# Kernel tuning notes

Hardware: AMD Instinct MI355X
Metric: run time of the kernel (lower is better)

The kernel has to match this reference:

```python
import jax, jax.numpy as jnp
import numpy as np

N, D = 4194304, 3  # points on S^2 embedded in R^3
STEPS = 100


def proj2tangent(x, v):
    # v - (<x,v>/<x,x>) x  : ambient projection onto tangent space at x
    dot = jnp.sum(x * v, axis=-1, keepdims=True)
    nrm2 = jnp.sum(x * x, axis=-1, keepdims=True)
    return v - (dot / nrm2) * x


def proj2manifold(x):
    return x / jnp.linalg.norm(x, axis=-1, keepdims=True)


def setup_inputs() -> dict:
    key = jax.random.key(0)
    x = jax.random.normal(key, (N, D), dtype=jnp.float32)
    x = proj2manifold(x)  # start on the sphere
    return {"x": x, "t": 1, "steps": STEPS}


def reference(x, t, steps):
    # Stratonovich-Heun integration of spherical Brownian motion.
    # drift f == 0; diffusion increment g(x, t, dW) = proj2tangent(x, dW).
    dt = t / steps
    sqrt_dt = jnp.sqrt(jnp.asarray(dt, dtype=x.dtype))
    base_key = jax.random.key(1)

    def step_fn(xc, i):
        inc = jax.random.normal(jax.random.fold_in(base_key, i), xc.shape, xc.dtype) * sqrt_dt
        g0 = proj2tangent(xc, inc)
        y_prime = xc + g0                     # f0 * dt == 0
        g_prime = proj2tangent(y_prime, inc)
        y1 = xc + 0.5 * (g0 + g_prime)        # 0.5*(f0+f')*dt == 0
        return proj2manifold(y1), None

    x_final, _ = jax.lax.scan(step_fn, x, jnp.arange(steps))
    return x_final
```

## Files before the change

kernel.cpp:

```cpp
#include <hip/hip_runtime.h>
#include <stdint.h>


#define BLOCK 256

struct V3 { float x, y, z; };

__device__ __forceinline__ void tf_round(uint32_t& x0, uint32_t& x1, int r) {
    x0 += x1;
    x1 = (x1 << r) | (x1 >> (32 - r));
    x1 ^= x0;
}

__device__ __forceinline__ uint2 threefry2x32(uint32_t k0, uint32_t k1,
                                              uint32_t x0, uint32_t x1) {
    uint32_t k2 = k0 ^ k1 ^ 0x1BD11BDAu;
    x0 += k0; x1 += k1;
    tf_round(x0,x1,13); tf_round(x0,x1,15); tf_round(x0,x1,26); tf_round(x0,x1,6);
    x0 += k1; x1 += k2 + 1u;
    tf_round(x0,x1,17); tf_round(x0,x1,29); tf_round(x0,x1,16); tf_round(x0,x1,24);
    x0 += k2; x1 += k0 + 2u;
    tf_round(x0,x1,13); tf_round(x0,x1,15); tf_round(x0,x1,26); tf_round(x0,x1,6);
    x0 += k0; x1 += k1 + 3u;
    tf_round(x0,x1,17); tf_round(x0,x1,29); tf_round(x0,x1,16); tf_round(x0,x1,24);
    x0 += k1; x1 += k2 + 4u;
    tf_round(x0,x1,13); tf_round(x0,x1,15); tf_round(x0,x1,26); tf_round(x0,x1,6);
    x0 += k2; x1 += k0 + 5u;
    return make_uint2(x0, x1);
}

__device__ __forceinline__ uint32_t tf_bits(uint32_t k0, uint32_t k1, uint32_t j) {
    uint2 h = threefry2x32(k0, k1, 0u, j);
    return h.x ^ h.y;
}

__device__ __forceinline__ float bits_to_inc(uint32_t bits, float c) {
    const float mn = -0.99999994f;
    float u01 = __uint_as_float((bits >> 9) | 0x3f800000u) - 1.0f;
    float u   = fmaf(u01, 2.0f, mn);
    float s   = u * u;
    float tt  = 1.0f - s;
    float w   = -__logf(tt);
    float wa  = w - 2.5f;
    float p =  2.81022636e-08f;
    p = fmaf(p, wa,  3.43273939e-07f);
    p = fmaf(p, wa, -3.5233877e-06f);
    p = fmaf(p, wa, -4.39150654e-06f);
    p = fmaf(p, wa,  0.00021858087f);
    p = fmaf(p, wa, -0.00125372503f);
    p = fmaf(p, wa, -0.00417768164f);
    p = fmaf(p, wa,  0.246640727f);
    p = fmaf(p, wa,  1.50140941f);
    if (__builtin_expect(__any(w >= 5.0f), 0)) {
        float wb = __builtin_amdgcn_sqrtf(w) - 3.0f;
        float q = -0.000200214257f;
        q = fmaf(q, wb,  0.000100950558f);
        q = fmaf(q, wb,  0.00134934322f);
        q = fmaf(q, wb, -0.00367342844f);
        q = fmaf(q, wb,  0.00573950773f);
        q = fmaf(q, wb, -0.0076224613f);
        q = fmaf(q, wb,  0.00943887047f);
        q = fmaf(q, wb,  1.00167406f);
        q = fmaf(q, wb,  2.83297682f);
        p = (w < 5.0f) ? p : q;
    }
    return (p * u) * c;
}

__device__ __forceinline__ float rcp_f(float a) { return __builtin_amdgcn_rcpf(a); }

__device__ __forceinline__ void heun_step(V3& p, V3 inc) {
    float d  = p.x*inc.x + p.y*inc.y + p.z*inc.z;
    float n2 = p.x*p.x + p.y*p.y + p.z*p.z;
    float q  = d * rcp_f(n2);
    V3 g0 = { inc.x - q*p.x, inc.y - q*p.y, inc.z - q*p.z };
    V3 yp = { p.x + g0.x, p.y + g0.y, p.z + g0.z };
    float d2 = yp.x*inc.x + yp.y*inc.y + yp.z*inc.z;
    float m2 = yp.x*yp.x + yp.y*yp.y + yp.z*yp.z;
    float q2 = d2 * rcp_f(m2);
    V3 gp = { inc.x - q2*yp.x, inc.y - q2*yp.y, inc.z - q2*yp.z };
    V3 y1 = { p.x + 0.5f*(g0.x+gp.x), p.y + 0.5f*(g0.y+gp.y), p.z + 0.5f*(g0.z+gp.z) };
    float r2   = y1.x*y1.x + y1.y*y1.y + y1.z*y1.z;
    float rinv = __builtin_amdgcn_rsqf(r2);
    p.x = y1.x * rinv; p.y = y1.y * rinv; p.z = y1.z * rinv;
}

__global__ __launch_bounds__(BLOCK)
void sbm_kernel(const float* __restrict__ xin,
                const int* __restrict__ t_ptr,
                const int* __restrict__ steps_ptr,
                float* __restrict__ out,
                uint32_t npts) {
    __shared__ uint2 skeys[128];

    const int steps = steps_ptr[0];
    const int tval  = t_ptr[0];
    const int tid   = threadIdx.x;

    if (tid < steps && tid < 128) skeys[tid] = threefry2x32(0u, 1u, 0u, (uint32_t)tid);
    __syncthreads();

    const float dt  = (float)((double)tval / (double)steps);
    const float sdt = sqrtf(dt);
    const float c   = 1.41421356237f * sdt;

    const uint32_t g = blockIdx.x * BLOCK + tid;
    if (g >= npts) return;

    const float* px = xin + 3u * g;
    V3 P = { px[0], px[1], px[2] };
    const uint32_t j0 = 3u * g;

    for (int i = 0; i < steps; ++i) {
        uint2 key = skeys[i & 127];
        uint32_t b0 = tf_bits(key.x, key.y, j0);
        uint32_t b1 = tf_bits(key.x, key.y, j0 + 1u);
        uint32_t b2 = tf_bits(key.x, key.y, j0 + 2u);
        V3 inc = { bits_to_inc(b0, c), bits_to_inc(b1, c), bits_to_inc(b2, c) };
        heun_step(P, inc);
    }

    float* po = out + 3u * g;
    po[0] = P.x; po[1] = P.y; po[2] = P.z;
}

extern "C" void kernel_launch(void* const* d_in, const int* in_sizes, int n_in,
                              void* d_out, int out_size, void* d_ws, size_t ws_size,
                              hipStream_t stream) {
    const float* x      = (const float*)d_in[0];
    const int*   t_ptr  = (const int*)d_in[1];
    const int*   steps  = (const int*)d_in[2];
    float*       out    = (float*)d_out;

    const uint32_t npts = (uint32_t)(in_sizes[0] / 3);
    const uint32_t grid = (npts + BLOCK - 1) / BLOCK;

    sbm_kernel<<<grid, BLOCK, 0, stream>>>(x, t_ptr, steps, out, npts);
}
```

Measured before the change: 2.836 ms.

## Process two points per thread, scalarize RNG keys, and simplify log and projection

Each thread now integrates two points, one from each half of the array, to expose more independent work per thread. The per-step Threefry key is broadcast with readfirstlane so the key arithmetic can live in scalar registers. The inverse-erf path uses log2 folded into an fma, and the first tangent projection drops the norm division on the assumption that the point is already unit length. This halves the thread count and silently leaves one point unprocessed if the point count is odd.

```diff
diff --git a/kernel.cpp b/kernel.cpp
--- a/kernel.cpp
+++ b/kernel.cpp
@@ -40,8 +40,9 @@
     float u   = fmaf(u01, 2.0f, mn);
     float s   = u * u;
     float tt  = 1.0f - s;
-    float w   = -__logf(tt);
-    float wa  = w - 2.5f;
+    float lg  = __log2f(tt);
+    const float nln2 = -0.69314718f;
+    float wa  = fmaf(lg, nln2, -2.5f);
     float p =  2.81022636e-08f;
     p = fmaf(p, wa,  3.43273939e-07f);
     p = fmaf(p, wa, -3.5233877e-06f);
@@ -51,7 +52,8 @@
     p = fmaf(p, wa, -0.00417768164f);
     p = fmaf(p, wa,  0.246640727f);
     p = fmaf(p, wa,  1.50140941f);
-    if (__builtin_expect(__any(w >= 5.0f), 0)) {
+    if (__builtin_expect(__any(lg <= -7.2134752f), 0)) {
+        float w  = lg * nln2;
         float wb = __builtin_amdgcn_sqrtf(w) - 3.0f;
         float q = -0.000200214257f;
         q = fmaf(q, wb,  0.000100950558f);
@@ -62,7 +64,7 @@
         q = fmaf(q, wb,  0.00943887047f);
         q = fmaf(q, wb,  1.00167406f);
         q = fmaf(q, wb,  2.83297682f);
-        p = (w < 5.0f) ? p : q;
+        p = (lg > -7.2134752f) ? p : q;
     }
     return (p * u) * c;
 }
@@ -71,9 +73,7 @@
 
 __device__ __forceinline__ void heun_step(V3& p, V3 inc) {
     float d  = p.x*inc.x + p.y*inc.y + p.z*inc.z;
-    float n2 = p.x*p.x + p.y*p.y + p.z*p.z;
-    float q  = d * rcp_f(n2);
-    V3 g0 = { inc.x - q*p.x, inc.y - q*p.y, inc.z - q*p.z };
+    V3 g0 = { inc.x - d*p.x, inc.y - d*p.y, inc.z - d*p.z };
     V3 yp = { p.x + g0.x, p.y + g0.y, p.z + g0.z };
     float d2 = yp.x*inc.x + yp.y*inc.y + yp.z*inc.z;
     float m2 = yp.x*yp.x + yp.y*yp.y + yp.z*yp.z;
@@ -90,7 +90,7 @@
                 const int* __restrict__ t_ptr,
                 const int* __restrict__ steps_ptr,
                 float* __restrict__ out,
-                uint32_t npts) {
+                uint32_t nhalf) {
     __shared__ uint2 skeys[128];
 
     const int steps = steps_ptr[0];
@@ -105,23 +105,35 @@
     const float c   = 1.41421356237f * sdt;
 
     const uint32_t g = blockIdx.x * BLOCK + tid;
-    if (g >= npts) return;
+    if (g >= nhalf) return;
 
-    const float* px = xin + 3u * g;
-    V3 P = { px[0], px[1], px[2] };
-    const uint32_t j0 = 3u * g;
+    const float* pa = xin + 3u * g;
+    const float* pb = xin + 3u * (g + nhalf);
+    V3 A = { pa[0], pa[1], pa[2] };
+    V3 B = { pb[0], pb[1], pb[2] };
+    const uint32_t ja = 3u * g;
+    const uint32_t jb = 3u * (g + nhalf);
 
     for (int i = 0; i < steps; ++i) {
         uint2 key = skeys[i & 127];
-        uint32_t b0 = tf_bits(key.x, key.y, j0);
-        uint32_t b1 = tf_bits(key.x, key.y, j0 + 1u);
-        uint32_t b2 = tf_bits(key.x, key.y, j0 + 2u);
-        V3 inc = { bits_to_inc(b0, c), bits_to_inc(b1, c), bits_to_inc(b2, c) };
-        heun_step(P, inc);
+        uint32_t k0 = __builtin_amdgcn_readfirstlane(key.x);
+        uint32_t k1 = __builtin_amdgcn_readfirstlane(key.y);
+        uint32_t a0 = tf_bits(k0, k1, ja);
+        uint32_t a1 = tf_bits(k0, k1, ja + 1u);
+        uint32_t a2 = tf_bits(k0, k1, ja + 2u);
+        uint32_t b0 = tf_bits(k0, k1, jb);
+        uint32_t b1 = tf_bits(k0, k1, jb + 1u);
+        uint32_t b2 = tf_bits(k0, k1, jb + 2u);
+        V3 incA = { bits_to_inc(a0, c), bits_to_inc(a1, c), bits_to_inc(a2, c) };
+        V3 incB = { bits_to_inc(b0, c), bits_to_inc(b1, c), bits_to_inc(b2, c) };
+        heun_step(A, incA);
+        heun_step(B, incB);
     }
 
-    float* po = out + 3u * g;
-    po[0] = P.x; po[1] = P.y; po[2] = P.z;
+    float* oa = out + 3u * g;
+    float* ob = out + 3u * (g + nhalf);
+    oa[0] = A.x; oa[1] = A.y; oa[2] = A.z;
+    ob[0] = B.x; ob[1] = B.y; ob[2] = B.z;
 }
 
 extern "C" void kernel_launch(void* const* d_in, const int* in_sizes, int n_in,
@@ -132,8 +144,9 @@
     const int*   steps  = (const int*)d_in[2];
     float*       out    = (float*)d_out;
 
-    const uint32_t npts = (uint32_t)(in_sizes[0] / 3);
-    const uint32_t grid = (npts + BLOCK - 1) / BLOCK;
+    const uint32_t npts  = (uint32_t)(in_sizes[0] / 3);
+    const uint32_t nhalf = npts / 2;
+    const uint32_t grid  = (nhalf + BLOCK - 1) / BLOCK;
 
-    sbm_kernel<<<grid, BLOCK, 0, stream>>>(x, t_ptr, steps, out, npts);
+    sbm_kernel<<<grid, BLOCK, 0, stream>>>(x, t_ptr, steps, out, nhalf);
 }
```

Result: faster. 2.706 ms (-4.6%).
